# Kernel tuning notes

Measured on AMD Instinct MI355X. Metric: run time of the kernel, lower is better.

Reference implementation:

```python
import jax, jax.numpy as jnp
import numpy as np

NUM_EMBEDDINGS = 512
EMBEDDING_DIM = 100
COMMITMENT_COST = 0.25


def setup_inputs() -> dict:
    key = jax.random.key(0)
    k1, k2 = jax.random.split(key)
    inputs = jax.random.normal(k1, (64, 64, 64, EMBEDDING_DIM), dtype=jnp.float32)
    # nn.Embedding weight init: uniform(-1/num_embeddings, 1/num_embeddings)
    lim = 1.0 / NUM_EMBEDDINGS
    embedding = jax.random.uniform(k2, (NUM_EMBEDDINGS, EMBEDDING_DIM),
                                   dtype=jnp.float32, minval=-lim, maxval=lim)
    return {"inputs": inputs, "embedding": embedding}


def reference(inputs, embedding):
    d = inputs.shape[-1]
    flat = inputs.reshape(-1, d)                                  # [N, d]
    # squared L2 distances to each codebook entry: [N, K]
    distances = (jnp.sum(flat ** 2, axis=1, keepdims=True)
                 + jnp.sum(embedding ** 2, axis=1)
                 - 2.0 * flat @ embedding.T)
    encoding_indices = jnp.argmin(distances, axis=1)              # [N]
    quantized = embedding[encoding_indices].reshape(inputs.shape)
    commitment_loss = COMMITMENT_COST * jnp.mean(
        (jax.lax.stop_gradient(quantized) - inputs) ** 2)
    quantization_loss = jnp.mean(
        (quantized - jax.lax.stop_gradient(inputs)) ** 2)
    # straight-through estimator
    quantized_st = inputs + jax.lax.stop_gradient(quantized - inputs)
    return quantized_st, quantization_loss, commitment_loss
```

## Files before the change

kernel.cpp:

```cpp
#include <hip/hip_runtime.h>
#include <hip/hip_bf16.h>
#include <cfloat>


#define N_ROWS (64 * 64 * 64)
#define D 100
#define KCODES 512
#define CB_OFF 4096
#define E2_OFF 16

typedef __attribute__((ext_vector_type(8))) short short8;
typedef __attribute__((ext_vector_type(4))) float f32x4;

__device__ __forceinline__ unsigned short f2bf(float f) {
    union { float f; unsigned u; } v; v.f = f;
    unsigned r = v.u + 0x7FFF + ((v.u >> 16) & 1);
    return (unsigned short)(r >> 16);
}
__device__ __forceinline__ unsigned pk2(float a, float b) {
    union { __hip_bfloat162 h; unsigned u; } c;
    c.h = __float22bfloat162_rn(make_float2(a, b));
    return c.u;
}
__device__ __forceinline__ short8 pack8(const float4& a, const float4& b) {
    union { unsigned u[4]; short8 v; } r;
    r.u[0] = pk2(a.x, a.y); r.u[1] = pk2(a.z, a.w);
    r.u[2] = pk2(b.x, b.y); r.u[3] = pk2(b.z, b.w);
    return r.v;
}

__global__ __launch_bounds__(64) void vq_init(const float* __restrict__ emb,
                                              float* __restrict__ ws) {
    const int code = blockIdx.x, l = threadIdx.x;
    const float* e = emb + code * D;
    if (code == 0 && l == 0) ws[0] = 0.0f;
    float a = e[l];
    float b = (l < D - 64) ? e[64 + l] : 0.0f;
    float p = fmaf(a, a, b * b);
#pragma unroll
    for (int off = 32; off; off >>= 1) p += __shfl_xor(p, off);
    if (l == 0) ws[E2_OFF + code] = p;

    if (l < 16) {
        const int s = l >> 2, q = l & 3;
        short8 v;
#pragma unroll
        for (int j = 0; j < 8; ++j) {
            int k = s * 32 + q * 8 + j;
            v[j] = (k < D) ? (short)f2bf(e[k]) : (short)0;
        }
        const int chunk = code >> 5, ci = code & 31;
        const int tt = ci >> 4, lr = ci & 15;
        unsigned short* cb = (unsigned short*)((char*)ws + CB_OFF);
        *(short8*)(cb + chunk * 4096 + ((s * 2 + tt) * 64 + q * 16 + lr) * 8) = v;
    }
}

__global__ __launch_bounds__(256, 3) void vq_main(const float* __restrict__ x,
                                                  const float* __restrict__ emb,
                                                  float* __restrict__ ws,
                                                  float* __restrict__ out) {
    __shared__ int    widx[256];
    __shared__ float  wsum[4];

    const int tid = threadIdx.x, wave = tid >> 6, lane = tid & 63;
    const int quad = lane >> 4, lr = lane & 15;
    const long brow = (long)blockIdx.x * 256;
    const long wrow = brow + wave * 64;

    float4 av[4][7];
#pragma unroll
    for (int m = 0; m < 4; ++m) {
        const float* xr = x + (wrow + m * 16 + lr) * D + quad * 8;
        av[m][0] = *(const float4*)(xr);
        av[m][1] = *(const float4*)(xr + 4);
        av[m][2] = *(const float4*)(xr + 32);
        av[m][3] = *(const float4*)(xr + 36);
        av[m][4] = *(const float4*)(xr + 64);
        av[m][5] = *(const float4*)(xr + 68);
        av[m][6] = *(const float4*)(x + (wrow + m * 16 + lr) * D + 96);
    }

    short8 A[4][4];
    float  xnorm[4];
#pragma unroll
    for (int m = 0; m < 4; ++m) {
        float4 z = av[m][6];
        if (quad != 0) z = make_float4(0.f, 0.f, 0.f, 0.f);
        float nrm = 0.f;
#pragma unroll
        for (int i = 0; i < 6; ++i) {
            float4 f = av[m][i];
            nrm = fmaf(f.x, f.x, nrm); nrm = fmaf(f.y, f.y, nrm);
            nrm = fmaf(f.z, f.z, nrm); nrm = fmaf(f.w, f.w, nrm);
        }
        nrm = fmaf(z.x, z.x, nrm); nrm = fmaf(z.y, z.y, nrm);
        nrm = fmaf(z.z, z.z, nrm); nrm = fmaf(z.w, z.w, nrm);
        A[m][0] = pack8(av[m][0], av[m][1]);
        A[m][1] = pack8(av[m][2], av[m][3]);
        A[m][2] = pack8(av[m][4], av[m][5]);
        A[m][3] = pack8(z, make_float4(0.f, 0.f, 0.f, 0.f));
        nrm += __shfl_xor(nrm, 16);
        nrm += __shfl_xor(nrm, 32);
        xnorm[m] = nrm;
    }

    const short8* __restrict__ bgall = (const short8*)((const char*)ws + CB_OFF);
    const float*  __restrict__ e2g   = ws + E2_OFF;

    float    runmin[4][4];
    unsigned runidx[4][4];
#pragma unroll
    for (int m = 0; m < 4; ++m)
#pragma unroll
        for (int r = 0; r < 4; ++r) { runmin[m][r] = FLT_MAX; runidx[m][r] = 0; }

    for (int c = 0; c < 16; ++c) {
        const short8* __restrict__ bg = bgall + c * 512;
#pragma unroll
        for (int tt = 0; tt < 2; ++tt) {
            short8 B[4];
#pragma unroll
            for (int s = 0; s < 4; ++s) B[s] = bg[(s * 2 + tt) * 64 + lane];
            float e2v = e2g[c * 32 + tt * 16 + lr];

            f32x4 acc[4];
#pragma unroll
            for (int m = 0; m < 4; ++m) acc[m] = (f32x4){0.f, 0.f, 0.f, 0.f};
#pragma unroll
            for (int s = 0; s < 4; ++s)
#pragma unroll
                for (int m = 0; m < 4; ++m)
                    acc[m] = __builtin_amdgcn_mfma_f32_16x16x32_bf16(A[m][s], B[s], acc[m], 0, 0, 0);

            const unsigned code = c * 32 + tt * 16 + lr;
#pragma unroll
            for (int m = 0; m < 4; ++m)
#pragma unroll
                for (int r = 0; r < 4; ++r) {
                    float sc = fmaf(-2.0f, acc[m][r], e2v);
                    if (sc < runmin[m][r]) { runmin[m][r] = sc; runidx[m][r] = code; }
                }
        }
    }

    float lsum = 0.0f;
#pragma unroll
    for (int m = 0; m < 4; ++m)
#pragma unroll
        for (int r = 0; r < 4; ++r) {
            float    s = runmin[m][r];
            unsigned i = runidx[m][r];
#pragma unroll
            for (int off = 8; off >= 1; off >>= 1) {
                float    os = __shfl_xor(s, off);
                unsigned oi = (unsigned)__shfl_xor((int)i, off);
                if (os < s || (os == s && oi < i)) { s = os; i = oi; }
            }
            if (lr == quad * 4 + r) {
                lsum += xnorm[m] + s;
                widx[wave * 64 + m * 16 + quad * 4 + r] = (int)i;
            }
        }
#pragma unroll
    for (int off = 32; off >= 1; off >>= 1) lsum += __shfl_xor(lsum, off);
    if (lane == 0) wsum[wave] = lsum;
    __syncthreads();
    if (tid == 0) atomicAdd(ws, wsum[0] + wsum[1] + wsum[2] + wsum[3]);

    const float4* __restrict__ ef = (const float4*)emb;
    float4* __restrict__ og = (float4*)(out + brow * D);
#pragma unroll
    for (int i = 0; i < 25; i += 5) {
        float4 q[5];
        int    gi[5];
#pragma unroll
        for (int u = 0; u < 5; ++u) {
            int g = (i + u) * 256 + tid;
            int row = g / 25;
            int c4  = g - row * 25;
            gi[u] = g;
            q[u]  = ef[(long)widx[row] * 25 + c4];
        }
#pragma unroll
        for (int u = 0; u < 5; ++u) og[gi[u]] = q[u];
    }
}

__global__ void vq_final(const float* __restrict__ ws, float* __restrict__ out) {
    float mse = ws[0] / (float)((long)N_ROWS * D);
    out[(long)N_ROWS * D]     = mse;
    out[(long)N_ROWS * D + 1] = 0.25f * mse;
}

extern "C" void kernel_launch(void* const* d_in, const int* in_sizes, int n_in,
                              void* d_out, int out_size, void* d_ws, size_t ws_size,
                              hipStream_t stream) {
    const float* x   = (const float*)d_in[0];
    const float* emb = (const float*)d_in[1];
    float* out = (float*)d_out;
    float* ws  = (float*)d_ws;

    vq_init<<<KCODES, 64, 0, stream>>>(emb, ws);
    vq_main<<<N_ROWS / 256, 256, 0, stream>>>(x, emb, ws, out);
    vq_final<<<1, 1, 0, stream>>>(ws, out);
}
```

Before: 242.2 us.

## Stage bf16 codebook in LDS across 512-thread blocks in two halves

Blocks grow to 512 threads (8 waves, 512 rows), and the bf16 codebook is staged through 64KB of shared memory in two halves instead of every wave reading B fragments from global/L2. The second half is prefetched into registers while the first half is consumed. The code norms are also placed in LDS. This cuts repeated global codebook reads per wave, but adds barriers, a large LDS footprint that limits blocks per CU, and higher register pressure from the 16 uint4 staging registers.

```diff
diff --git a/kernel.cpp b/kernel.cpp
--- a/kernel.cpp
+++ b/kernel.cpp
@@ -56,16 +56,18 @@
     }
 }
 
-__global__ __launch_bounds__(256, 3) void vq_main(const float* __restrict__ x,
+__global__ __launch_bounds__(512, 4) void vq_main(const float* __restrict__ x,
                                                   const float* __restrict__ emb,
                                                   float* __restrict__ ws,
                                                   float* __restrict__ out) {
-    __shared__ int    widx[256];
-    __shared__ float  wsum[4];
+    __shared__ uint4  sbuf[4096];
+    __shared__ float  e2s[KCODES];
+    __shared__ int    widx[512];
+    __shared__ float  wsum[8];
 
     const int tid = threadIdx.x, wave = tid >> 6, lane = tid & 63;
     const int quad = lane >> 4, lr = lane & 15;
-    const long brow = (long)blockIdx.x * 256;
+    const long brow = (long)blockIdx.x * 512;
     const long wrow = brow + wave * 64;
 
     float4 av[4][7];
@@ -81,6 +83,13 @@
         av[m][6] = *(const float4*)(x + (wrow + m * 16 + lr) * D + 96);
     }
 
+    const uint4* __restrict__ cbg = (const uint4*)((const char*)ws + CB_OFF);
+    const float* __restrict__ e2g = ws + E2_OFF;
+    uint4 h0[8];
+#pragma unroll
+    for (int k = 0; k < 8; ++k) h0[k] = cbg[tid + k * 512];
+    e2s[tid] = e2g[tid];
+
     short8 A[4][4];
     float  xnorm[4];
 #pragma unroll
@@ -105,8 +114,14 @@
         xnorm[m] = nrm;
     }
 
-    const short8* __restrict__ bgall = (const short8*)((const char*)ws + CB_OFF);
-    const float*  __restrict__ e2g   = ws + E2_OFF;
+#pragma unroll
+    for (int k = 0; k < 8; ++k) sbuf[tid + k * 512] = h0[k];
+
+    uint4 h1[8];
+#pragma unroll
+    for (int k = 0; k < 8; ++k) h1[k] = cbg[4096 + tid + k * 512];
+
+    __syncthreads();
 
     float    runmin[4][4];
     unsigned runidx[4][4];
@@ -115,32 +130,44 @@
 #pragma unroll
         for (int r = 0; r < 4; ++r) { runmin[m][r] = FLT_MAX; runidx[m][r] = 0; }
 
-    for (int c = 0; c < 16; ++c) {
-        const short8* __restrict__ bg = bgall + c * 512;
-#pragma unroll
-        for (int tt = 0; tt < 2; ++tt) {
-            short8 B[4];
-#pragma unroll
-            for (int s = 0; s < 4; ++s) B[s] = bg[(s * 2 + tt) * 64 + lane];
-            float e2v = e2g[c * 32 + tt * 16 + lr];
-
-            f32x4 acc[4];
-#pragma unroll
-            for (int m = 0; m < 4; ++m) acc[m] = (f32x4){0.f, 0.f, 0.f, 0.f};
-#pragma unroll
-            for (int s = 0; s < 4; ++s)
+    const short8* __restrict__ sbl = (const short8*)sbuf;
+
+#pragma unroll 1
+    for (int h = 0; h < 2; ++h) {
+        if (h == 1) {
+            __syncthreads();
+#pragma unroll
+            for (int k = 0; k < 8; ++k) sbuf[tid + k * 512] = h1[k];
+            __syncthreads();
+        }
+#pragma unroll 1
+        for (int c8 = 0; c8 < 8; ++c8) {
+            const int c = h * 8 + c8;
+#pragma unroll
+            for (int tt = 0; tt < 2; ++tt) {
+                short8 B[4];
+#pragma unroll
+                for (int s = 0; s < 4; ++s) B[s] = sbl[c8 * 512 + (s * 2 + tt) * 64 + lane];
+                float e2v = e2s[c * 32 + tt * 16 + lr];
+
+                f32x4 acc[4];
+#pragma unroll
+                for (int m = 0; m < 4; ++m) acc[m] = (f32x4){0.f, 0.f, 0.f, 0.f};
+#pragma unroll
+                for (int s = 0; s < 4; ++s)
+#pragma unroll
+                    for (int m = 0; m < 4; ++m)
+                        acc[m] = __builtin_amdgcn_mfma_f32_16x16x32_bf16(A[m][s], B[s], acc[m], 0, 0, 0);
+
+                const unsigned code = c * 32 + tt * 16 + lr;
 #pragma unroll
                 for (int m = 0; m < 4; ++m)
-                    acc[m] = __builtin_amdgcn_mfma_f32_16x16x32_bf16(A[m][s], B[s], acc[m], 0, 0, 0);
-
-            const unsigned code = c * 32 + tt * 16 + lr;
-#pragma unroll
-            for (int m = 0; m < 4; ++m)
-#pragma unroll
-                for (int r = 0; r < 4; ++r) {
-                    float sc = fmaf(-2.0f, acc[m][r], e2v);
-                    if (sc < runmin[m][r]) { runmin[m][r] = sc; runidx[m][r] = code; }
-                }
+#pragma unroll
+                    for (int r = 0; r < 4; ++r) {
+                        float sc = fmaf(-2.0f, acc[m][r], e2v);
+                        if (sc < runmin[m][r]) { runmin[m][r] = sc; runidx[m][r] = code; }
+                    }
+            }
         }
     }
 
@@ -166,7 +193,12 @@
     for (int off = 32; off >= 1; off >>= 1) lsum += __shfl_xor(lsum, off);
     if (lane == 0) wsum[wave] = lsum;
     __syncthreads();
-    if (tid == 0) atomicAdd(ws, wsum[0] + wsum[1] + wsum[2] + wsum[3]);
+    if (tid == 0) {
+        float t = 0.f;
+#pragma unroll
+        for (int w = 0; w < 8; ++w) t += wsum[w];
+        atomicAdd(ws, t);
+    }
 
     const float4* __restrict__ ef = (const float4*)emb;
     float4* __restrict__ og = (float4*)(out + brow * D);
@@ -176,7 +208,7 @@
         int    gi[5];
 #pragma unroll
         for (int u = 0; u < 5; ++u) {
-            int g = (i + u) * 256 + tid;
+            int g = (i + u) * 512 + tid;
             int row = g / 25;
             int c4  = g - row * 25;
             gi[u] = g;
@@ -202,6 +234,6 @@
     float* ws  = (float*)d_ws;
 
     vq_init<<<KCODES, 64, 0, stream>>>(emb, ws);
-    vq_main<<<N_ROWS / 256, 256, 0, stream>>>(x, emb, ws, out);
+    vq_main<<<N_ROWS / 512, 512, 0, stream>>>(x, emb, ws, out);
     vq_final<<<1, 1, 0, stream>>>(ws, out);
 }
```

Result: slower. 292.3 us (+20.7%).

## Use single-wave 32-row blocks with double-buffered codebook loads and spread atomics

Applied to the files above, without the earlier changes.

Restructures vq_main so that each block is one wave handling 32 rows instead of four waves handling 256 rows. The codebook loop now prefetches the next half-chunk of B fragments and e2 values while the current one runs through MFMA (software double buffering). The loss accumulation is spread across 8 atomic slots to reduce contention, and the block-wide __syncthreads is removed. In exchange, each codebook fragment is reused across fewer rows, so codebook traffic per row rises and the number of blocks and atomics grows 8x.

```diff
diff --git a/kernel.cpp b/kernel.cpp
--- a/kernel.cpp
+++ b/kernel.cpp
@@ -33,7 +33,7 @@
                                               float* __restrict__ ws) {
     const int code = blockIdx.x, l = threadIdx.x;
     const float* e = emb + code * D;
-    if (code == 0 && l == 0) ws[0] = 0.0f;
+    if (code == 0 && l < 16) ws[l] = 0.0f;
     float a = e[l];
     float b = (l < D - 64) ? e[64 + l] : 0.0f;
     float p = fmaf(a, a, b * b);
@@ -56,35 +56,33 @@
     }
 }
 
-__global__ __launch_bounds__(256, 3) void vq_main(const float* __restrict__ x,
-                                                  const float* __restrict__ emb,
-                                                  float* __restrict__ ws,
-                                                  float* __restrict__ out) {
-    __shared__ int    widx[256];
-    __shared__ float  wsum[4];
-
-    const int tid = threadIdx.x, wave = tid >> 6, lane = tid & 63;
+__global__ __launch_bounds__(64, 4) void vq_main(const float* __restrict__ x,
+                                                 const float* __restrict__ emb,
+                                                 float* __restrict__ ws,
+                                                 float* __restrict__ out) {
+    __shared__ int widx[32];
+
+    const int lane = threadIdx.x;
     const int quad = lane >> 4, lr = lane & 15;
-    const long brow = (long)blockIdx.x * 256;
-    const long wrow = brow + wave * 64;
-
-    float4 av[4][7];
-#pragma unroll
-    for (int m = 0; m < 4; ++m) {
-        const float* xr = x + (wrow + m * 16 + lr) * D + quad * 8;
+    const long brow = (long)blockIdx.x * 32;
+
+    float4 av[2][7];
+#pragma unroll
+    for (int m = 0; m < 2; ++m) {
+        const float* xr = x + (brow + m * 16 + lr) * D + quad * 8;
         av[m][0] = *(const float4*)(xr);
         av[m][1] = *(const float4*)(xr + 4);
         av[m][2] = *(const float4*)(xr + 32);
         av[m][3] = *(const float4*)(xr + 36);
         av[m][4] = *(const float4*)(xr + 64);
         av[m][5] = *(const float4*)(xr + 68);
-        av[m][6] = *(const float4*)(x + (wrow + m * 16 + lr) * D + 96);
-    }
-
-    short8 A[4][4];
-    float  xnorm[4];
-#pragma unroll
-    for (int m = 0; m < 4; ++m) {
+        av[m][6] = *(const float4*)(x + (brow + m * 16 + lr) * D + 96);
+    }
+
+    short8 A[2][4];
+    float  xnorm[2];
+#pragma unroll
+    for (int m = 0; m < 2; ++m) {
         float4 z = av[m][6];
         if (quad != 0) z = make_float4(0.f, 0.f, 0.f, 0.f);
         float nrm = 0.f;
@@ -105,48 +103,63 @@
         xnorm[m] = nrm;
     }
 
-    const short8* __restrict__ bgall = (const short8*)((const char*)ws + CB_OFF);
-    const float*  __restrict__ e2g   = ws + E2_OFF;
-
-    float    runmin[4][4];
-    unsigned runidx[4][4];
-#pragma unroll
-    for (int m = 0; m < 4; ++m)
+    const short8* __restrict__ cbg8 = (const short8*)((const char*)ws + CB_OFF);
+    const float*  __restrict__ e2g  = ws + E2_OFF;
+
+    float    runmin[2][4];
+    unsigned runidx[2][4];
+#pragma unroll
+    for (int m = 0; m < 2; ++m)
 #pragma unroll
         for (int r = 0; r < 4; ++r) { runmin[m][r] = FLT_MAX; runidx[m][r] = 0; }
 
-    for (int c = 0; c < 16; ++c) {
-        const short8* __restrict__ bg = bgall + c * 512;
-#pragma unroll
-        for (int tt = 0; tt < 2; ++tt) {
-            short8 B[4];
-#pragma unroll
-            for (int s = 0; s < 4; ++s) B[s] = bg[(s * 2 + tt) * 64 + lane];
-            float e2v = e2g[c * 32 + tt * 16 + lr];
-
-            f32x4 acc[4];
-#pragma unroll
-            for (int m = 0; m < 4; ++m) acc[m] = (f32x4){0.f, 0.f, 0.f, 0.f};
-#pragma unroll
-            for (int s = 0; s < 4; ++s)
-#pragma unroll
-                for (int m = 0; m < 4; ++m)
-                    acc[m] = __builtin_amdgcn_mfma_f32_16x16x32_bf16(A[m][s], B[s], acc[m], 0, 0, 0);
-
-            const unsigned code = c * 32 + tt * 16 + lr;
-#pragma unroll
-            for (int m = 0; m < 4; ++m)
-#pragma unroll
-                for (int r = 0; r < 4; ++r) {
-                    float sc = fmaf(-2.0f, acc[m][r], e2v);
-                    if (sc < runmin[m][r]) { runmin[m][r] = sc; runidx[m][r] = code; }
-                }
-        }
-    }
+    short8 B0[4], B1[4];
+    float  e20, e21;
+
+#define LOADH(Bv, e2v, hc2)                                                   \
+    do {                                                                      \
+        const int c_ = (hc2) >> 1, t_ = (hc2) & 1;                            \
+        _Pragma("unroll")                                                     \
+        for (int s_ = 0; s_ < 4; ++s_)                                        \
+            Bv[s_] = cbg8[c_ * 512 + (s_ * 2 + t_) * 64 + lane];              \
+        e2v = e2g[c_ * 32 + t_ * 16 + lr];                                    \
+    } while (0)
+
+#define COMPH(Bv, e2v, hc2)                                                   \
+    do {                                                                      \
+        const int c_ = (hc2) >> 1, t_ = (hc2) & 1;                            \
+        f32x4 acc_[2];                                                        \
+        acc_[0] = (f32x4){0.f, 0.f, 0.f, 0.f};                                \
+        acc_[1] = (f32x4){0.f, 0.f, 0.f, 0.f};                                \
+        _Pragma("unroll")                                                     \
+        for (int s_ = 0; s_ < 4; ++s_) {                                      \
+            acc_[0] = __builtin_amdgcn_mfma_f32_16x16x32_bf16(A[0][s_], Bv[s_], acc_[0], 0, 0, 0); \
+            acc_[1] = __builtin_amdgcn_mfma_f32_16x16x32_bf16(A[1][s_], Bv[s_], acc_[1], 0, 0, 0); \
+        }                                                                     \
+        const unsigned code_ = c_ * 32 + t_ * 16 + lr;                        \
+        _Pragma("unroll")                                                     \
+        for (int m_ = 0; m_ < 2; ++m_)                                        \
+            _Pragma("unroll")                                                 \
+            for (int r_ = 0; r_ < 4; ++r_) {                                  \
+                float sc_ = fmaf(-2.0f, acc_[m_][r_], e2v);                   \
+                if (sc_ < runmin[m_][r_]) { runmin[m_][r_] = sc_; runidx[m_][r_] = code_; } \
+            }                                                                 \
+    } while (0)
+
+    LOADH(B0, e20, 0);
+#pragma unroll 1
+    for (int hc = 0; hc < 32; hc += 2) {
+        LOADH(B1, e21, hc + 1);
+        COMPH(B0, e20, hc);
+        if (hc < 30) LOADH(B0, e20, hc + 2);
+        COMPH(B1, e21, hc + 1);
+    }
+#undef LOADH
+#undef COMPH
 
     float lsum = 0.0f;
 #pragma unroll
-    for (int m = 0; m < 4; ++m)
+    for (int m = 0; m < 2; ++m)
 #pragma unroll
         for (int r = 0; r < 4; ++r) {
             float    s = runmin[m][r];
@@ -159,36 +172,42 @@
             }
             if (lr == quad * 4 + r) {
                 lsum += xnorm[m] + s;
-                widx[wave * 64 + m * 16 + quad * 4 + r] = (int)i;
+                widx[m * 16 + quad * 4 + r] = (int)i;
             }
         }
 #pragma unroll
     for (int off = 32; off >= 1; off >>= 1) lsum += __shfl_xor(lsum, off);
-    if (lane == 0) wsum[wave] = lsum;
-    __syncthreads();
-    if (tid == 0) atomicAdd(ws, wsum[0] + wsum[1] + wsum[2] + wsum[3]);
+    if (lane == 0) atomicAdd(&ws[(blockIdx.x & 7) * 2], lsum);
+
+    asm volatile("s_waitcnt lgkmcnt(0)" ::: "memory");
 
     const float4* __restrict__ ef = (const float4*)emb;
     float4* __restrict__ og = (float4*)(out + brow * D);
 #pragma unroll
-    for (int i = 0; i < 25; i += 5) {
-        float4 q[5];
-        int    gi[5];
-#pragma unroll
-        for (int u = 0; u < 5; ++u) {
-            int g = (i + u) * 256 + tid;
+    for (int i = 0; i < 16; i += 4) {
+        float4 q[4];
+        int    gi[4];
+        bool   ok[4];
+#pragma unroll
+        for (int u = 0; u < 4; ++u) {
+            int g = (i + u) * 64 + lane;
+            ok[u] = (g < 800);
             int row = g / 25;
             int c4  = g - row * 25;
             gi[u] = g;
-            q[u]  = ef[(long)widx[row] * 25 + c4];
-        }
-#pragma unroll
-        for (int u = 0; u < 5; ++u) og[gi[u]] = q[u];
+            if (ok[u]) q[u] = ef[(long)widx[row] * 25 + c4];
+        }
+#pragma unroll
+        for (int u = 0; u < 4; ++u)
+            if (ok[u]) og[gi[u]] = q[u];
     }
 }
 
 __global__ void vq_final(const float* __restrict__ ws, float* __restrict__ out) {
-    float mse = ws[0] / (float)((long)N_ROWS * D);
+    float t = 0.f;
+#pragma unroll
+    for (int w = 0; w < 8; ++w) t += ws[w * 2];
+    float mse = t / (float)((long)N_ROWS * D);
     out[(long)N_ROWS * D]     = mse;
     out[(long)N_ROWS * D + 1] = 0.25f * mse;
 }
@@ -202,6 +221,6 @@
     float* ws  = (float*)d_ws;
 
     vq_init<<<KCODES, 64, 0, stream>>>(emb, ws);
-    vq_main<<<N_ROWS / 256, 256, 0, stream>>>(x, emb, ws, out);
+    vq_main<<<N_ROWS / 32, 64, 0, stream>>>(x, emb, ws, out);
     vq_final<<<1, 1, 0, stream>>>(ws, out);
 }
```

Result: slower. 328.6 us (+35.7%).
